# Kernel tuning notes

Hardware: AMD Instinct MI355X
Metric: run time of the kernel (lower is better)

## Reference

```python
import jax, jax.numpy as jnp
import numpy as np

N_NODES = 50000
N_EDGES = 800000
IN_DIM = 128
OUT_DIM = 64


def setup_inputs() -> dict:
    key = jax.random.key(0)
    k1, k2, k3, k4, k5 = jax.random.split(key, 5)
    x = jax.random.normal(k1, (N_NODES, IN_DIM), dtype=jnp.float32)
    # Glorot-uniform-ish init for the GCN weight (weight_variable_glorot)
    limit = np.sqrt(6.0 / (IN_DIM + OUT_DIM)).astype(np.float32)
    weight = jax.random.uniform(k2, (IN_DIM, OUT_DIM), dtype=jnp.float32,
                                minval=-limit, maxval=limit)
    adj_row = jax.random.randint(k3, (N_EDGES,), 0, N_NODES, dtype=jnp.int32)
    adj_col = jax.random.randint(k4, (N_EDGES,), 0, N_NODES, dtype=jnp.int32)
    adj_val = jax.random.uniform(k5, (N_EDGES,), dtype=jnp.float32)
    return {"x": x, "weight": weight, "adj_row": adj_row,
            "adj_col": adj_col, "adj_val": adj_val}


def reference(x, weight, adj_row, adj_col, adj_val):
    # x: [N, F_in], weight: [F_in, F_out]; dropout=0.0 (default) is identity.
    xw = jnp.matmul(x, weight)                      # [N, F_out] dense GEMM
    # spmm(adj, xw) with adj in COO: gather neighbor feats, scale, scatter-add
    msg = adj_val[:, None] * xw[adj_col]            # [E, F_out]
    agg = jax.ops.segment_sum(msg, adj_row, num_segments=x.shape[0])  # [N, F_out]
    return jax.nn.relu(agg)
```

## Files before the change

### kernel.cpp

```cpp
#include <hip/hip_runtime.h>

#define IN_DIM 128
#define OUT_DIM 64
#define PADK 136
#define RB 64
#define RBSH 6
#define CAPB 1280
#define AB2 128

typedef float f32x4 __attribute__((ext_vector_type(4)));
typedef short bf16x8 __attribute__((ext_vector_type(8)));

__device__ __forceinline__ unsigned short f2bf(float f) {
    unsigned u = __float_as_uint(f);
    return (unsigned short)((u + 0x7FFFu + ((u >> 16) & 1u)) >> 16);
}
__device__ __forceinline__ float bf2f(unsigned short h) {
    return __uint_as_float((unsigned)h << 16);
}

__device__ __forceinline__ void gemm_body(const float* __restrict__ x,
                                          const float* __restrict__ w,
                                          unsigned short* __restrict__ xwb,
                                          int N, int blk,
                                          unsigned short* lds) {
    unsigned short* Ahi = lds;
    unsigned short* Alo = lds + 64 * PADK;
    unsigned short* Bhi = lds + 2 * 64 * PADK;
    unsigned short* Blo = lds + 3 * 64 * PADK;

    const int t = threadIdx.x;
    const int r0 = blk * 64;

    {
        const int c = t >> 2;
        const int kb = (t & 3) * 32;
        for (int k4 = 0; k4 < 32; k4 += 4) {
            ushort4 h, l;
            float v0 = w[(kb + k4 + 0) * OUT_DIM + c];
            float v1 = w[(kb + k4 + 1) * OUT_DIM + c];
            float v2 = w[(kb + k4 + 2) * OUT_DIM + c];
            float v3 = w[(kb + k4 + 3) * OUT_DIM + c];
            h.x = f2bf(v0); l.x = f2bf(v0 - bf2f(h.x));
            h.y = f2bf(v1); l.y = f2bf(v1 - bf2f(h.y));
            h.z = f2bf(v2); l.z = f2bf(v2 - bf2f(h.z));
            h.w = f2bf(v3); l.w = f2bf(v3 - bf2f(h.w));
            *(ushort4*)&Bhi[c * PADK + kb + k4] = h;
            *(ushort4*)&Blo[c * PADK + kb + k4] = l;
        }
    }
    {
        const float4* x4 = (const float4*)x;
        for (int i = 0; i < 8; ++i) {
            const int f = i * 256 + t;
            const int rr = f >> 5;
            const int kk = (f & 31) * 4;
            int row = r0 + rr; if (row >= N) row = N - 1;
            float4 v = x4[(size_t)row * (IN_DIM / 4) + (kk >> 2)];
            ushort4 h, l;
            h.x = f2bf(v.x); l.x = f2bf(v.x - bf2f(h.x));
            h.y = f2bf(v.y); l.y = f2bf(v.y - bf2f(h.y));
            h.z = f2bf(v.z); l.z = f2bf(v.z - bf2f(h.z));
            h.w = f2bf(v.w); l.w = f2bf(v.w - bf2f(h.w));
            *(ushort4*)&Ahi[rr * PADK + kk] = h;
            *(ushort4*)&Alo[rr * PADK + kk] = l;
        }
    }
    __syncthreads();

    const int lane = t & 63;
    const int wv = t >> 6;
    const int m = lane & 15;
    const int quad = lane >> 4;

    bf16x8 ahi[4], alo[4];
#pragma unroll
    for (int ks = 0; ks < 4; ++ks) {
        const int off = (wv * 16 + m) * PADK + ks * 32 + quad * 8;
        ahi[ks] = *(const bf16x8*)&Ahi[off];
        alo[ks] = *(const bf16x8*)&Alo[off];
    }
#pragma unroll
    for (int ct = 0; ct < 4; ++ct) {
        f32x4 acc = {0.f, 0.f, 0.f, 0.f};
#pragma unroll
        for (int ks = 0; ks < 4; ++ks) {
            const int off = (ct * 16 + m) * PADK + ks * 32 + quad * 8;
            bf16x8 bh = *(const bf16x8*)&Bhi[off];
            bf16x8 bl = *(const bf16x8*)&Blo[off];
            acc = __builtin_amdgcn_mfma_f32_16x16x32_bf16(alo[ks], bh, acc, 0, 0, 0);
            acc = __builtin_amdgcn_mfma_f32_16x16x32_bf16(ahi[ks], bl, acc, 0, 0, 0);
            acc = __builtin_amdgcn_mfma_f32_16x16x32_bf16(ahi[ks], bh, acc, 0, 0, 0);
        }
#pragma unroll
        for (int i = 0; i < 4; ++i) {
            const int row = r0 + wv * 16 + quad * 4 + i;
            if (row < N) xwb[(size_t)row * OUT_DIM + ct * 16 + m] = f2bf(acc[i]);
        }
    }
}

__device__ __forceinline__ void afill_body(
        const int* __restrict__ arow, const int* __restrict__ acol,
        const float* __restrict__ aval, int* __restrict__ pcur,
        int* __restrict__ ocount, uint4* __restrict__ olist,
        uint2* __restrict__ payload, int E, int NB, int chunk, int blk,
        int* ldsi) {
    int* cnt  = ldsi;
    int* base = ldsi + 1024;
    const int t = threadIdx.x;
    const int lo = blk * chunk;
    const int hi = min(E, lo + chunk);
    if (lo >= hi) return;
    for (int i = t; i < NB; i += 256) cnt[i] = 0;
    __syncthreads();
    for (int e = lo + t; e < hi; e += 256)
        atomicAdd(&cnt[arow[e] >> RBSH], 1);
    __syncthreads();
    for (int i = t; i < NB; i += 256) {
        const int c = cnt[i];
        base[i] = c ? atomicAdd(&pcur[i], c) : 0;
        cnt[i] = 0;
    }
    __syncthreads();
    for (int e = lo + t; e < hi; e += 256) {
        const int r = arow[e];
        const int b = r >> RBSH;
        const int slot = base[b] + atomicAdd(&cnt[b], 1);
        const unsigned w0 = (unsigned)acol[e] | ((unsigned)(r & (RB - 1)) << 16);
        const unsigned w1 = __float_as_uint(aval[e]);
        if (slot < CAPB) {
            payload[(size_t)b * CAPB + slot] = make_uint2(w0, w1);
        } else {
            const int oi = atomicAdd(ocount, 1);
            olist[oi] = make_uint4((unsigned)r, (unsigned)acol[e], w1, 0u);
        }
    }
}

__global__ __launch_bounds__(256) void gemm_afill(
        const float* __restrict__ x, const float* __restrict__ w,
        unsigned short* __restrict__ xwb, int N,
        const int* __restrict__ arow, const int* __restrict__ acol,
        const float* __restrict__ aval, int* __restrict__ pcur,
        int* __restrict__ ocount, uint4* __restrict__ olist,
        uint2* __restrict__ payload, int E, int NB, int chunk) {
    __shared__ unsigned short LB[4 * 64 * PADK];
    if ((int)blockIdx.x < AB2) {
        afill_body(arow, acol, aval, pcur, ocount, olist, payload, E, NB,
                   chunk, blockIdx.x, (int*)LB);
    } else {
        gemm_body(x, w, xwb, N, blockIdx.x - AB2, LB);
    }
}

__global__ __launch_bounds__(256) void gemm_only(const float* __restrict__ x,
                                                 const float* __restrict__ w,
                                                 unsigned short* __restrict__ xwb,
                                                 int N) {
    __shared__ unsigned short LB[4 * 64 * PADK];
    gemm_body(x, w, xwb, N, blockIdx.x, LB);
}

__global__ __launch_bounds__(512) void bagg3(
        const int* __restrict__ pcur, const uint2* __restrict__ payload,
        const unsigned short* __restrict__ xwb, float* __restrict__ out, int N,
        const int* __restrict__ ocount, const uint4* __restrict__ olist) {
    __shared__ uint2 stage[CAPB];
    __shared__ int bins[RB + 1];
    __shared__ int pl[RB];
    const int t = threadIdx.x;
    const int lane = t & 63;
    const int wv = t >> 6;
    const int b = blockIdx.x;
    const int r0 = b << RBSH;

    const int cnt = min(pcur[b], CAPB);
    if (t <= RB) bins[t] = 0;
    if (t < RB) pl[t] = 0;
    __syncthreads();

    const uint2* pay = payload + (size_t)b * CAPB;
    for (int i = t; i < cnt; i += 512)
        atomicAdd(&bins[(pay[i].x >> 16) & (RB - 1)], 1);
    __syncthreads();
    if (t == 0) {
        int run = 0;
        for (int i = 0; i < RB; ++i) { int v = bins[i]; bins[i] = run; run += v; }
        bins[RB] = run;
    }
    __syncthreads();
    for (int i = t; i < cnt; i += 512) {
        const uint2 e = pay[i];
        const int rl = (e.x >> 16) & (RB - 1);
        stage[bins[rl] + atomicAdd(&pl[rl], 1)] = e;
    }
    __syncthreads();

    float acc[8];
#pragma unroll
    for (int lr = 0; lr < 8; ++lr) {
        const int row = wv * 8 + lr;
        int j = bins[row];
        const int end = bins[row + 1];
        float a0 = 0.f, a1 = 0.f;
        for (; j + 8 <= end; j += 8) {
            uint2 e0 = stage[j],   e1 = stage[j+1], e2 = stage[j+2], e3 = stage[j+3];
            uint2 e4 = stage[j+4], e5 = stage[j+5], e6 = stage[j+6], e7 = stage[j+7];
            float g0 = bf2f(xwb[(size_t)(e0.x & 0xFFFF) * OUT_DIM + lane]);
            float g1 = bf2f(xwb[(size_t)(e1.x & 0xFFFF) * OUT_DIM + lane]);
            float g2 = bf2f(xwb[(size_t)(e2.x & 0xFFFF) * OUT_DIM + lane]);
            float g3 = bf2f(xwb[(size_t)(e3.x & 0xFFFF) * OUT_DIM + lane]);
            float g4 = bf2f(xwb[(size_t)(e4.x & 0xFFFF) * OUT_DIM + lane]);
            float g5 = bf2f(xwb[(size_t)(e5.x & 0xFFFF) * OUT_DIM + lane]);
            float g6 = bf2f(xwb[(size_t)(e6.x & 0xFFFF) * OUT_DIM + lane]);
            float g7 = bf2f(xwb[(size_t)(e7.x & 0xFFFF) * OUT_DIM + lane]);
            a0 = fmaf(__uint_as_float(e0.y), g0, a0);
            a1 = fmaf(__uint_as_float(e1.y), g1, a1);
            a0 = fmaf(__uint_as_float(e2.y), g2, a0);
            a1 = fmaf(__uint_as_float(e3.y), g3, a1);
            a0 = fmaf(__uint_as_float(e4.y), g4, a0);
            a1 = fmaf(__uint_as_float(e5.y), g5, a1);
            a0 = fmaf(__uint_as_float(e6.y), g6, a0);
            a1 = fmaf(__uint_as_float(e7.y), g7, a1);
        }
        for (; j + 4 <= end; j += 4) {
            uint2 e0 = stage[j], e1 = stage[j+1], e2 = stage[j+2], e3 = stage[j+3];
            float g0 = bf2f(xwb[(size_t)(e0.x & 0xFFFF) * OUT_DIM + lane]);
            float g1 = bf2f(xwb[(size_t)(e1.x & 0xFFFF) * OUT_DIM + lane]);
            float g2 = bf2f(xwb[(size_t)(e2.x & 0xFFFF) * OUT_DIM + lane]);
            float g3 = bf2f(xwb[(size_t)(e3.x & 0xFFFF) * OUT_DIM + lane]);
            a0 = fmaf(__uint_as_float(e0.y), g0, a0);
            a1 = fmaf(__uint_as_float(e1.y), g1, a1);
            a0 = fmaf(__uint_as_float(e2.y), g2, a0);
            a1 = fmaf(__uint_as_float(e3.y), g3, a1);
        }
        for (; j < end; ++j) {
            uint2 e0 = stage[j];
            a0 = fmaf(__uint_as_float(e0.y),
                      bf2f(xwb[(size_t)(e0.x & 0xFFFF) * OUT_DIM + lane]), a0);
        }
        acc[lr] = a0 + a1;
    }

    const int oc = *ocount;
    for (int i = 0; i < oc; ++i) {
        const uint4 e = olist[i];
        const int lr = (int)e.x - r0 - wv * 8;
        if (lr >= 0 && lr < 8)
            acc[lr] += __uint_as_float(e.z) *
                       bf2f(xwb[(size_t)e.y * OUT_DIM + lane]);
    }

#pragma unroll
    for (int lr = 0; lr < 8; ++lr) {
        const int row = r0 + wv * 8 + lr;
        if (row < N) {
            const float v = acc[lr];
            out[(size_t)row * OUT_DIM + lane] = v > 0.f ? v : 0.f;
        }
    }
}

__global__ __launch_bounds__(256) void scatter_edges(
        const int* __restrict__ arow, const int* __restrict__ acol,
        const float* __restrict__ aval, const unsigned short* __restrict__ xwb,
        float* __restrict__ out, int E) {
    const int lane = threadIdx.x & 63;
    int gw = (blockIdx.x * 256 + (int)threadIdx.x) >> 6;
    const int nw = (gridDim.x * 256) >> 6;
    for (int e = gw; e < E; e += nw) {
        const float m = aval[e] * bf2f(xwb[(size_t)acol[e] * OUT_DIM + lane]);
        atomicAdd(&out[(size_t)arow[e] * OUT_DIM + lane], m);
    }
}

__global__ __launch_bounds__(256) void relu_inplace(float* __restrict__ o, int n4) {
    float4* p = (float4*)o;
    int i = blockIdx.x * 256 + threadIdx.x;
    const int stride = gridDim.x * 256;
    for (; i < n4; i += stride) {
        float4 v = p[i];
        v.x = v.x > 0.f ? v.x : 0.f;
        v.y = v.y > 0.f ? v.y : 0.f;
        v.z = v.z > 0.f ? v.z : 0.f;
        v.w = v.w > 0.f ? v.w : 0.f;
        p[i] = v;
    }
}

static inline size_t align256(size_t x) { return (x + 255) & ~(size_t)255; }

extern "C" void kernel_launch(void* const* d_in, const int* in_sizes, int n_in,
                              void* d_out, int out_size, void* d_ws, size_t ws_size,
                              hipStream_t stream) {
    const float* x    = (const float*)d_in[0];
    const float* w    = (const float*)d_in[1];
    const int*   arow = (const int*)d_in[2];
    const int*   acol = (const int*)d_in[3];
    const float* aval = (const float*)d_in[4];
    float*       out  = (float*)d_out;

    const int N  = in_sizes[0] / IN_DIM;
    const int E  = in_sizes[2];
    const int NB = (N + RB - 1) >> RBSH;
    const int GB = (N + 63) / 64;

    char* ws = (char*)d_ws;
    const size_t szXW  = align256((size_t)N * OUT_DIM * sizeof(unsigned short));
    const size_t szCnt = align256((size_t)(NB + 1) * sizeof(int));
    const size_t szOl  = align256((size_t)E * sizeof(uint4));
    const size_t szPay = (size_t)NB * CAPB * sizeof(uint2);
    const size_t need0 = szXW + szCnt + szOl + szPay;

    unsigned short* xwb = (unsigned short*)ws;
    int*   pcur    = (int*)(ws + szXW);
    int*   ocount  = pcur + NB;
    uint4* olist   = (uint4*)(ws + szXW + szCnt);
    uint2* payload = (uint2*)(ws + szXW + szCnt + szOl);

    if (ws_size >= need0 && N <= 65536 && NB <= 1024) {
        (void)hipMemsetAsync(pcur, 0, (size_t)(NB + 1) * sizeof(int), stream);
        const int chunk = (E + AB2 - 1) / AB2;
        gemm_afill<<<AB2 + GB, 256, 0, stream>>>(x, w, xwb, N, arow, acol, aval,
                                                 pcur, ocount, olist, payload,
                                                 E, NB, chunk);
        bagg3<<<NB, 512, 0, stream>>>(pcur, payload, xwb, out, N, ocount, olist);
    } else {
        gemm_only<<<GB, 256, 0, stream>>>(x, w, xwb, N);
        (void)hipMemsetAsync(d_out, 0, (size_t)out_size * sizeof(float), stream);
        scatter_edges<<<4096, 256, 0, stream>>>(arow, acol, aval, xwb, out, E);
        relu_inplace<<<2048, 256, 0, stream>>>(out, out_size / 4);
    }
}
```

Baseline: 129.9 us.

## Vectorize edge-fill loads, double fill blocks, parallelize row-bin prefix scan

The edge-binning pass now reads row, col and value arrays as 128-bit vectors, four edges per thread iteration, with the chunk rounded to a multiple of four so each chunk stays aligned. The number of fill blocks doubles from 128 to 256, giving more parallelism alongside the GEMM blocks. The serial single-thread prefix sum over the 64 row bins in the aggregation kernel becomes a wavefront shuffle scan. The cost is more global atomics on the per-bucket cursors, and the order of entries within each bucket changes.

```diff
diff --git a/kernel.cpp b/kernel.cpp
--- a/kernel.cpp
+++ b/kernel.cpp
@@ -6,7 +6,7 @@
 #define RB 64
 #define RBSH 6
 #define CAPB 1280
-#define AB2 128
+#define AB2 256
 
 typedef float f32x4 __attribute__((ext_vector_type(4)));
 typedef short bf16x8 __attribute__((ext_vector_type(8)));
@@ -112,30 +112,59 @@
     const int lo = blk * chunk;
     const int hi = min(E, lo + chunk);
     if (lo >= hi) return;
+    const int len = hi - lo;
+    const int n4  = len >> 2;
+    const int4*   ar4 = (const int4*)(arow + lo);
+    const int4*   ac4 = (const int4*)(acol + lo);
+    const float4* av4 = (const float4*)(aval + lo);
+
     for (int i = t; i < NB; i += 256) cnt[i] = 0;
     __syncthreads();
-    for (int e = lo + t; e < hi; e += 256)
+
+    for (int j = t; j < n4; j += 256) {
+        const int4 r = ar4[j];
+        atomicAdd(&cnt[r.x >> RBSH], 1);
+        atomicAdd(&cnt[r.y >> RBSH], 1);
+        atomicAdd(&cnt[r.z >> RBSH], 1);
+        atomicAdd(&cnt[r.w >> RBSH], 1);
+    }
+    for (int e = lo + (n4 << 2) + t; e < hi; e += 256)
         atomicAdd(&cnt[arow[e] >> RBSH], 1);
     __syncthreads();
+
     for (int i = t; i < NB; i += 256) {
         const int c = cnt[i];
         base[i] = c ? atomicAdd(&pcur[i], c) : 0;
         cnt[i] = 0;
     }
     __syncthreads();
-    for (int e = lo + t; e < hi; e += 256) {
-        const int r = arow[e];
-        const int b = r >> RBSH;
-        const int slot = base[b] + atomicAdd(&cnt[b], 1);
-        const unsigned w0 = (unsigned)acol[e] | ((unsigned)(r & (RB - 1)) << 16);
-        const unsigned w1 = __float_as_uint(aval[e]);
-        if (slot < CAPB) {
-            payload[(size_t)b * CAPB + slot] = make_uint2(w0, w1);
-        } else {
-            const int oi = atomicAdd(ocount, 1);
-            olist[oi] = make_uint4((unsigned)r, (unsigned)acol[e], w1, 0u);
-        }
-    }
+
+#define AF_EMIT(RR, CC, VV) do {                                              \
+        const int b_ = (RR) >> RBSH;                                          \
+        const int slot_ = base[b_] + atomicAdd(&cnt[b_], 1);                  \
+        const unsigned w0_ = (unsigned)(CC) |                                 \
+                             ((unsigned)((RR) & (RB - 1)) << 16);             \
+        const unsigned w1_ = __float_as_uint(VV);                             \
+        if (slot_ < CAPB) {                                                   \
+            payload[(size_t)b_ * CAPB + slot_] = make_uint2(w0_, w1_);        \
+        } else {                                                              \
+            const int oi_ = atomicAdd(ocount, 1);                             \
+            olist[oi_] = make_uint4((unsigned)(RR), (unsigned)(CC), w1_, 0u); \
+        }                                                                     \
+    } while (0)
+
+    for (int j = t; j < n4; j += 256) {
+        const int4   r = ar4[j];
+        const int4   c = ac4[j];
+        const float4 v = av4[j];
+        AF_EMIT(r.x, c.x, v.x);
+        AF_EMIT(r.y, c.y, v.y);
+        AF_EMIT(r.z, c.z, v.z);
+        AF_EMIT(r.w, c.w, v.w);
+    }
+    for (int e = lo + (n4 << 2) + t; e < hi; e += 256)
+        AF_EMIT(arow[e], acol[e], aval[e]);
+#undef AF_EMIT
 }
 
 __global__ __launch_bounds__(256) void gemm_afill(
@@ -184,10 +213,16 @@
     for (int i = t; i < cnt; i += 512)
         atomicAdd(&bins[(pay[i].x >> 16) & (RB - 1)], 1);
     __syncthreads();
-    if (t == 0) {
-        int run = 0;
-        for (int i = 0; i < RB; ++i) { int v = bins[i]; bins[i] = run; run += v; }
-        bins[RB] = run;
+    if (t < RB) {
+        const int v = bins[t];
+        int s = v;
+#pragma unroll
+        for (int d = 1; d < RB; d <<= 1) {
+            const int u = __shfl_up(s, d, 64);
+            if (t >= d) s += u;
+        }
+        bins[t + 1] = s;
+        if (t == 0) bins[0] = 0;
     }
     __syncthreads();
     for (int i = t; i < cnt; i += 512) {
@@ -321,7 +356,7 @@
 
     if (ws_size >= need0 && N <= 65536 && NB <= 1024) {
         (void)hipMemsetAsync(pcur, 0, (size_t)(NB + 1) * sizeof(int), stream);
-        const int chunk = (E + AB2 - 1) / AB2;
+        const int chunk = (((E + AB2 - 1) / AB2) + 3) & ~3;
         gemm_afill<<<AB2 + GB, 256, 0, stream>>>(x, w, xwb, N, arow, acol, aval,
                                                  pcur, ocount, olist, payload,
                                                  E, NB, chunk);
```

Measured after the change: 123.5 us, median of 2. 4.9% less time.
